# Kernel tuning notes

Hardware: AMD Instinct MI355X
Metric: run time of the kernel (lower is better)

Reference implementation:

```python
import jax, jax.numpy as jnp
import numpy as np
import math

B, LQ, D = 4, 1024, 2048
H, G = 16, 4            # n_heads, n_groups
HD = D // H             # 128
GS = H // G             # group_size = 4
PAST = 1024
LK = PAST + LQ
NEG = jnp.float32(-1e30)


def _rope(x, cos, sin):
    # x: [B, L, nh, HD]; cos/sin: [1, L, 1, HD//2]; llama-style complex rotation
    x1 = x[..., 0::2]
    x2 = x[..., 1::2]
    r1 = x1 * cos - x2 * sin
    r2 = x1 * sin + x2 * cos
    return jnp.stack([r1, r2], axis=-1).reshape(x.shape)


def setup_inputs() -> dict:
    key = jax.random.key(0)
    ks = jax.random.split(key, 12)
    s = 0.02
    x = jax.random.normal(ks[0], (B, LQ, D), jnp.float32)
    past_k = jax.random.normal(ks[1], (B, G, PAST, HD), jnp.float32)
    past_v = jax.random.normal(ks[2], (B, G, PAST, HD), jnp.float32)
    rotary_freqs = jax.random.uniform(ks[3], (LQ, HD // 2), jnp.float32) * 6.283
    # causal mask with cache: query i may attend to key j if j <= PAST + i
    q_pos = PAST + jnp.arange(LQ)[:, None]
    k_pos = jnp.arange(LK)[None, :]
    mask = (k_pos <= q_pos)  # [LQ, LK] bool
    Wq = jax.random.normal(ks[4], (D, D), jnp.float32) * s
    bq = jnp.zeros((D,), jnp.float32)
    Wk = jax.random.normal(ks[5], (D, G * HD), jnp.float32) * s
    bk = jnp.zeros((G * HD,), jnp.float32)
    Wv = jax.random.normal(ks[6], (D, G * HD), jnp.float32) * s
    bv = jnp.zeros((G * HD,), jnp.float32)
    Wo = jax.random.normal(ks[7], (D, D), jnp.float32) * s
    bo = jnp.zeros((D,), jnp.float32)
    return {"x": x, "mask": mask, "rotary_freqs": rotary_freqs,
            "past_k": past_k, "past_v": past_v,
            "Wq": Wq, "bq": bq, "Wk": Wk, "bk": bk,
            "Wv": Wv, "bv": bv, "Wo": Wo, "bo": bo}


def reference(x, mask, rotary_freqs, past_k, past_v, Wq, bq, Wk, bk, Wv, bv, Wo, bo):
    # projections (torch Linear math with weights stored [in, out])
    q = (x @ Wq + bq).reshape(B, LQ, H, HD)      # break_heads: [B,L,H,HD]
    k = (x @ Wk + bk).reshape(B, LQ, G, HD)      # [B,L,G,HD]
    v = (x @ Wv + bv).reshape(B, LQ, G, HD).transpose(0, 2, 1, 3)  # [B,G,L,HD]
    # RoPE on q,k then move heads forward (matches q.transpose(2,1))
    cos = jnp.cos(rotary_freqs)[None, :, None, :]
    sin = jnp.sin(rotary_freqs)[None, :, None, :]
    q = _rope(q, cos, sin).transpose(0, 2, 1, 3)  # [B,H,LQ,HD]
    k = _rope(k, cos, sin).transpose(0, 2, 1, 3)  # [B,G,LQ,HD]
    # KV cache append
    k = jnp.concatenate([past_k, k], axis=2)      # [B,G,LK,HD]
    v = jnp.concatenate([past_v, v], axis=2)
    # grouped-query attention
    qg = q.reshape(B, G, GS, LQ, HD)
    scores = jnp.einsum('bgsqd,bgkd->bgsqk', qg, k) / math.sqrt(HD)
    scores = jnp.where(mask[None, None, None, :, :], scores, NEG)
    att = jax.nn.softmax(scores, axis=-1)
    out = jnp.einsum('bgsqk,bgkd->bgsqd', att, v).reshape(B, H, LQ, HD)
    out = out.transpose(0, 2, 1, 3).reshape(B, LQ, D)  # concatenate_heads
    return out @ Wo + bo
```

## Files before the change

kernel.cpp:

```cpp
#include <hip/hip_runtime.h>

#define B_   4
#define LQ_  1024
#define D_   2048
#define H_   16
#define G_   4
#define HD_  128
#define GS_  4
#define PAST_ 1024
#define LK_  2048
#define NQKV 3072

typedef __attribute__((ext_vector_type(8))) short short8;
typedef __attribute__((ext_vector_type(4))) float f32x4;

__device__ __forceinline__ ushort f2b(float f) {
    unsigned u = __builtin_bit_cast(unsigned, f);
    u += 0x7FFF + ((u >> 16) & 1);
    return (ushort)(u >> 16);
}
__device__ __forceinline__ float b2f(ushort h) {
    unsigned u = ((unsigned)h) << 16;
    return __builtin_bit_cast(float, u);
}

#define GLD_LDS16(gp, lp) \
    __builtin_amdgcn_global_load_lds((__attribute__((address_space(1))) void*)(gp), \
                                     (__attribute__((address_space(3))) void*)(lp), 16, 0, 0)

__global__ __launch_bounds__(256) void prep_misc(const float* __restrict__ x,
                                                 ushort* __restrict__ xb,
                                                 const float* __restrict__ pk,
                                                 ushort* __restrict__ kc,
                                                 const float* __restrict__ bq,
                                                 const float* __restrict__ bk,
                                                 const float* __restrict__ bv,
                                                 float* __restrict__ bias) {
    int blk = blockIdx.x;
    int tid = threadIdx.x;
    if (blk < 8192) {
        int i = blk * 256 + tid;
        float4 v = ((const float4*)x)[i];
        ushort4 o;
        o.x = f2b(v.x); o.y = f2b(v.y); o.z = f2b(v.z); o.w = f2b(v.w);
        ((ushort4*)xb)[i] = o;
    } else if (blk < 10240) {
        int i = (blk - 8192) * 256 + tid;
        float4 v = ((const float4*)pk)[i];
        int bg  = i >> 15;
        int rem = i & 32767;
        ushort4 o;
        o.x = f2b(v.x); o.y = f2b(v.y); o.z = f2b(v.z); o.w = f2b(v.w);
        ((ushort4*)kc)[(size_t)bg * 65536 + rem] = o;
    } else {
        int i = (blk - 10240) * 256 + tid;
        if (i < 2048) bias[i] = bq[i];
        else if (i < 2560) bias[i] = bk[i - 2048];
        else if (i < 3072) bias[i] = bv[i - 2560];
    }
}

__global__ __launch_bounds__(256) void transpose_pack(const float* __restrict__ in,
                                                      ushort* __restrict__ out,
                                                      int rows_in, int cols_in,
                                                      long in_bstride, long out_bstride,
                                                      int out_rstride) {
    __shared__ float t[32][33];
    int bz = blockIdx.z;
    in  += (long)bz * in_bstride;
    out += (long)bz * out_bstride;
    int c0 = blockIdx.x * 32, r0 = blockIdx.y * 32;
    int tx = threadIdx.x, ty = threadIdx.y;
    #pragma unroll
    for (int i = 0; i < 32; i += 8) {
        int r = r0 + ty + i;
        if (r < rows_in && (c0 + tx) < cols_in)
            t[ty + i][tx] = in[(long)r * cols_in + c0 + tx];
    }
    __syncthreads();
    #pragma unroll
    for (int i = 0; i < 32; i += 8) {
        int c = c0 + ty + i, r = r0 + tx;
        if (c < cols_in && r < rows_in)
            out[(long)c * out_rstride + r] = f2b(t[tx][ty + i]);
    }
}

template <bool BF16_OUT>
__global__ __launch_bounds__(512, 2) void gemm256(const ushort* __restrict__ Ap,
                                                  const ushort* __restrict__ Bp,
                                                  const float* __restrict__ bias,
                                                  void* __restrict__ Cout,
                                                  int M, int N, int K) {
    __shared__ ushort sh[65536];
    const int tid = threadIdx.x;
    const int w = tid >> 6, lane = tid & 63;
    const int quad = lane >> 4, l15 = lane & 15;
    const int wr = w >> 2, wc = w & 3;
    const int m0 = blockIdx.y * 256, n0 = blockIdx.x * 256;

    const int u0 = w * 64 + lane, u1 = (8 + w) * 64 + lane;
    const int r0_ = u0 >> 3, s0_ = u0 & 7;
    const int r1_ = u1 >> 3, s1_ = u1 & 7;
    const int sw0 = (s0_ ^ (r0_ & 7)) << 3, sw1 = (s1_ ^ (r1_ & 7)) << 3;
    const int srcA00 = (m0 + r0_) * K + sw0;
    const int srcA01 = (m0 + r1_) * K + sw1;
    const int srcA10 = (m0 + 128 + r0_) * K + sw0;
    const int srcA11 = (m0 + 128 + r1_) * K + sw1;
    const int srcB00 = (n0 + r0_) * K + sw0;
    const int srcB01 = (n0 + r1_) * K + sw1;
    const int srcB10 = (n0 + 128 + r0_) * K + sw0;
    const int srcB11 = (n0 + 128 + r1_) * K + sw1;

#define STAGE_A0(t, bufx) do { ushort* d_ = sh + (bufx) * 32768 + w * 512; \
    GLD_LDS16(Ap + (size_t)(srcA00 + (t) * 64), d_); \
    GLD_LDS16(Ap + (size_t)(srcA01 + (t) * 64), d_ + 4096); } while (0)
#define STAGE_A1(t, bufx) do { ushort* d_ = sh + (bufx) * 32768 + 8192 + w * 512; \
    GLD_LDS16(Ap + (size_t)(srcA10 + (t) * 64), d_); \
    GLD_LDS16(Ap + (size_t)(srcA11 + (t) * 64), d_ + 4096); } while (0)
#define STAGE_B0(t, bufx) do { ushort* d_ = sh + (bufx) * 32768 + 16384 + w * 512; \
    GLD_LDS16(Bp + (size_t)(srcB00 + (t) * 64), d_); \
    GLD_LDS16(Bp + (size_t)(srcB01 + (t) * 64), d_ + 4096); } while (0)
#define STAGE_B1(t, bufx) do { ushort* d_ = sh + (bufx) * 32768 + 16384 + 8192 + w * 512; \
    GLD_LDS16(Bp + (size_t)(srcB10 + (t) * 64), d_); \
    GLD_LDS16(Bp + (size_t)(srcB11 + (t) * 64), d_ + 4096); } while (0)

#define READ_A(QR) \
    _Pragma("unroll") for (int fi = 0; fi < 4; ++fi) \
    _Pragma("unroll") for (int ks = 0; ks < 2; ++ks) \
        a[fi * 2 + ks] = *(const short8*)(Ab + (wr * 128 + (QR) * 64 + fi * 16 + l15) * 64 + \
                                          (((ks * 4 + quad) ^ (l15 & 7)) << 3));
#define READ_B(QC, BREG) \
    _Pragma("unroll") for (int fj = 0; fj < 2; ++fj) \
    _Pragma("unroll") for (int ks = 0; ks < 2; ++ks) \
        BREG[fj * 2 + ks] = *(const short8*)(Bb + (wc * 64 + (QC) * 32 + fj * 16 + l15) * 64 + \
                                             (((ks * 4 + quad) ^ (l15 & 7)) << 3));
#define MFMA_Q(QR, QC, BREG) \
    _Pragma("unroll") for (int ks = 0; ks < 2; ++ks) \
    _Pragma("unroll") for (int fj = 0; fj < 2; ++fj) \
    _Pragma("unroll") for (int fi = 0; fi < 4; ++fi) \
        acc[(QR) * 4 + fi][(QC) * 2 + fj] = __builtin_amdgcn_mfma_f32_16x16x32_bf16( \
            a[fi * 2 + ks], BREG[fj * 2 + ks], acc[(QR) * 4 + fi][(QC) * 2 + fj], 0, 0, 0);

#define PH_MID() do { asm volatile("" ::: "memory"); __builtin_amdgcn_s_barrier(); \
    asm volatile("s_waitcnt lgkmcnt(0)" ::: "memory"); __builtin_amdgcn_sched_barrier(0); \
    __builtin_amdgcn_s_setprio(1); } while (0)
#define PH_END() do { __builtin_amdgcn_s_setprio(0); asm volatile("" ::: "memory"); \
    __builtin_amdgcn_s_barrier(); asm volatile("" ::: "memory"); } while (0)

    f32x4 acc[8][4];
    #pragma unroll
    for (int i = 0; i < 8; ++i)
        #pragma unroll
        for (int j = 0; j < 4; ++j)
            #pragma unroll
            for (int r = 0; r < 4; ++r) acc[i][j][r] = 0.f;

    const int KT = K >> 6;

    STAGE_A0(0, 0); STAGE_A1(0, 0); STAGE_B0(0, 0); STAGE_B1(0, 0);
    STAGE_B0(1, 1); STAGE_B1(1, 1);
    asm volatile("s_waitcnt vmcnt(4)" ::: "memory");
    asm volatile("" ::: "memory");
    __builtin_amdgcn_s_barrier();
    asm volatile("" ::: "memory");

    short8 a[8], b0[4], b1[4];
    for (int t = 0; t < KT; ++t) {
        const int buf = t & 1;
        const ushort* Ab = sh + buf * 32768;
        const ushort* Bb = Ab + 16384;

        READ_A(0)
        READ_B(0, b0)
        if (t + 1 < KT) STAGE_A0(t + 1, buf ^ 1);
        PH_MID();
        MFMA_Q(0, 0, b0)
        PH_END();

        READ_B(1, b1)
        if (t + 1 < KT) STAGE_A1(t + 1, buf ^ 1);
        PH_MID();
        MFMA_Q(0, 1, b1)
        PH_END();

        READ_A(1)
        if (t + 2 < KT) STAGE_B0(t + 2, buf);
        PH_MID();
        MFMA_Q(1, 0, b0)
        PH_END();

        if (t + 2 < KT) {
            STAGE_B1(t + 2, buf);
            asm volatile("s_waitcnt vmcnt(4)" ::: "memory");
        } else {
            asm volatile("s_waitcnt vmcnt(0)" ::: "memory");
        }
        PH_MID();
        MFMA_Q(1, 1, b1)
        PH_END();
    }

    #pragma unroll
    for (int fi = 0; fi < 8; ++fi)
        #pragma unroll
        for (int fj = 0; fj < 4; ++fj)
            #pragma unroll
            for (int r = 0; r < 4; ++r) {
                int row = m0 + wr * 128 + fi * 16 + quad * 4 + r;
                int col = n0 + wc * 64 + fj * 16 + l15;
                float v = acc[fi][fj][r] + bias[col];
                if (BF16_OUT) ((ushort*)Cout)[(size_t)row * N + col] = f2b(v);
                else          ((float*)Cout)[(size_t)row * N + col] = v;
            }
#undef STAGE_A0
#undef STAGE_A1
#undef STAGE_B0
#undef STAGE_B1
#undef READ_A
#undef READ_B
#undef MFMA_Q
#undef PH_MID
#undef PH_END
}

__global__ __launch_bounds__(256) void rope_pack(const ushort* __restrict__ qkvb,
                                                 const float* __restrict__ rf,
                                                 ushort* __restrict__ qb,
                                                 ushort* __restrict__ kc,
                                                 ushort* __restrict__ vtc) {
    const float SC = 0.08838834764831845f;
    int row = blockIdx.x;
    int b = row >> 10, qi = row & 1023;
    int tid = threadIdx.x;
    const ushort* src = qkvb + (size_t)row * NQKV;

    for (int p = tid; p < 1024; p += 256) {
        int h = p >> 6, i = p & 63;
        float fr = rf[qi * 64 + i];
        float s, c; __sincosf(fr, &s, &c);
        uint pr = *(const uint*)(src + h * 128 + 2 * i);
        float x1 = b2f((ushort)(pr & 0xffff));
        float x2 = b2f((ushort)(pr >> 16));
        float r1 = (x1 * c - x2 * s) * SC;
        float r2 = (x1 * s + x2 * c) * SC;
        size_t o = (((size_t)(b * H_ + h)) * LQ_ + qi) * HD_ + 2 * i;
        *(uint*)(qb + o) = (uint)f2b(r1) | ((uint)f2b(r2) << 16);
    }
    {
        int g = tid >> 6, i = tid & 63;
        float fr = rf[qi * 64 + i];
        float s, c; __sincosf(fr, &s, &c);
        uint pr = *(const uint*)(src + 2048 + g * 128 + 2 * i);
        float x1 = b2f((ushort)(pr & 0xffff));
        float x2 = b2f((ushort)(pr >> 16));
        float r1 = x1 * c - x2 * s;
        float r2 = x1 * s + x2 * c;
        size_t o = (((size_t)(b * G_ + g)) * LK_ + PAST_ + qi) * HD_ + 2 * i;
        *(uint*)(kc + o) = (uint)f2b(r1) | ((uint)f2b(r2) << 16);
    }
    for (int e = tid; e < 512; e += 256) {
        int g = e >> 7, d = e & 127;
        vtc[(((size_t)(b * G_ + g)) * HD_ + d) * LK_ + PAST_ + qi] = src[2560 + e];
    }
}

__global__ __launch_bounds__(256, 2) void attn_kernel(const ushort* __restrict__ qb,
                                                      const ushort* __restrict__ kc,
                                                      const ushort* __restrict__ vtc,
                                                      ushort* __restrict__ attn_a) {
    __shared__ ushort kt[2][64 * 128];
    __shared__ ushort vtt[2][128 * 64];
    __shared__ ushort pt[128 * 64];

    const int tid = threadIdx.x;
    const int wave = tid >> 6, lane = tid & 63;
    const int quad = lane >> 4, l15 = lane & 15;
    const int qh = wave >> 1;
    const int jw = wave & 1;
    const int tile = (blockIdx.y < 32) ? blockIdx.x : (7 - (int)blockIdx.x);
    const int q0 = tile << 7;
    const int bh = blockIdx.y;
    const int b = bh >> 4, h = bh & 15, g = h >> 2;
    const ushort* kcb = kc + ((size_t)(b * G_ + g)) * LK_ * HD_;
    const ushort* vcb = vtc + ((size_t)(b * G_ + g)) * HD_ * LK_;

    int ksrc[4], vsrc[4];
    #pragma unroll
    for (int i = 0; i < 4; ++i) {
        int u = (wave * 4 + i) * 64 + lane;
        int key = u >> 4, cs = u & 15;
        ksrc[i] = key * HD_ + ((cs ^ (key & 15)) << 3);
        int d = u >> 3, c2 = u & 7;
        vsrc[i] = d * LK_ + ((c2 ^ (d & 7)) << 3);
    }

    short8 qf[4][4];
    #pragma unroll
    for (int qfr = 0; qfr < 4; ++qfr) {
        int qrow = q0 + qh * 64 + qfr * 16 + l15;
        const ushort* qp = qb + (((size_t)(b * H_ + h)) * LQ_ + qrow) * HD_ + quad * 8;
        #pragma unroll
        for (int kk = 0; kk < 4; ++kk) qf[qfr][kk] = *(const short8*)(qp + kk * 32);
    }

    f32x4 o[4][4];
    #pragma unroll
    for (int qfr = 0; qfr < 4; ++qfr)
        #pragma unroll
        for (int f = 0; f < 4; ++f)
            #pragma unroll
            for (int r = 0; r < 4; ++r) o[qfr][f][r] = 0.f;
    float lst[4][4];
    #pragma unroll
    for (int qfr = 0; qfr < 4; ++qfr)
        #pragma unroll
        for (int r = 0; r < 4; ++r) lst[qfr][r] = 0.f;

    const int nsteps = (PAST_ + q0 + 128) >> 6;

    #pragma unroll
    for (int i = 0; i < 4; ++i) {
        int ci = wave * 4 + i;
        GLD_LDS16(kcb + ksrc[i], kt[0] + ci * 512);
        GLD_LDS16(vcb + vsrc[i], vtt[0] + ci * 512);
    }

    for (int it = 0; it < nsteps; ++it) {
        const int k0 = it << 6;
        const int cur = it & 1, nxt = cur ^ 1;
        __syncthreads();
        if (it + 1 < nsteps) {
            const int k1 = k0 + 64;
            #pragma unroll
            for (int i = 0; i < 4; ++i) {
                int ci = wave * 4 + i;
                GLD_LDS16(kcb + (size_t)k1 * HD_ + ksrc[i], kt[nxt] + ci * 512);
                GLD_LDS16(vcb + k1 + vsrc[i], vtt[nxt] + ci * 512);
            }
        }

        f32x4 z[4][2];
        #pragma unroll
        for (int qfr = 0; qfr < 4; ++qfr)
            #pragma unroll
            for (int kf = 0; kf < 2; ++kf)
                #pragma unroll
                for (int r = 0; r < 4; ++r) z[qfr][kf][r] = 0.f;
        __builtin_amdgcn_s_setprio(1);
        #pragma unroll
        for (int kk = 0; kk < 4; ++kk) {
            #pragma unroll
            for (int kf = 0; kf < 2; ++kf) {
                int key = jw * 32 + kf * 16 + l15;
                const short8 bk = *(const short8*)(kt[cur] + key * 128 + (((kk * 4 + quad) ^ l15) << 3));
                #pragma unroll
                for (int qfr = 0; qfr < 4; ++qfr)
                    z[qfr][kf] = __builtin_amdgcn_mfma_f32_16x16x32_bf16(qf[qfr][kk], bk, z[qfr][kf], 0, 0, 0);
            }
        }
        __builtin_amdgcn_s_setprio(0);

        const bool mask_step = (it >= nsteps - 2);
        #pragma unroll
        for (int qfr = 0; qfr < 4; ++qfr) {
            #pragma unroll
            for (int kf = 0; kf < 2; ++kf) {
                #pragma unroll
                for (int r = 0; r < 4; ++r) {
                    int row = qh * 64 + qfr * 16 + quad * 4 + r;
                    int col = jw * 32 + kf * 16 + l15;
                    float pv_ = __expf(z[qfr][kf][r]);
                    if (mask_step) {
                        int qpos = PAST_ + q0 + row;
                        if (k0 + col > qpos) pv_ = 0.f;
                    }
                    lst[qfr][r] += pv_;
                    pt[row * 64 + ((((col >> 3) ^ (row & 7)) << 3) | (col & 7))] = f2b(pv_);
                }
            }
        }

        asm volatile("s_waitcnt lgkmcnt(0)" ::: "memory");
        __builtin_amdgcn_s_barrier();
        __builtin_amdgcn_sched_barrier(0);

        __builtin_amdgcn_s_setprio(1);
        #pragma unroll
        for (int j2 = 0; j2 < 2; ++j2) {
            short8 pa[4];
            #pragma unroll
            for (int qfr = 0; qfr < 4; ++qfr) {
                int prow = qh * 64 + qfr * 16 + l15;
                pa[qfr] = *(const short8*)(pt + prow * 64 + (((j2 * 4 + quad) ^ (prow & 7)) << 3));
            }
            #pragma unroll
            for (int f = 0; f < 4; ++f) {
                int d = jw * 64 + f * 16 + l15;
                const short8 bv = *(const short8*)(vtt[cur] + d * 64 + (((j2 * 4 + quad) ^ (l15 & 7)) << 3));
                #pragma unroll
                for (int qfr = 0; qfr < 4; ++qfr)
                    o[qfr][f] = __builtin_amdgcn_mfma_f32_16x16x32_bf16(pa[qfr], bv, o[qfr][f], 0, 0, 0);
            }
        }
        __builtin_amdgcn_s_setprio(0);
    }

    __syncthreads();
    float* scr = (float*)pt;
    #pragma unroll
    for (int qfr = 0; qfr < 4; ++qfr)
        #pragma unroll
        for (int r = 0; r < 4; ++r)
            scr[wave * 1024 + (qfr * 4 + r) * 64 + lane] = lst[qfr][r];
    __syncthreads();
    #pragma unroll
    for (int qfr = 0; qfr < 4; ++qfr) {
        float linv[4];
        #pragma unroll
        for (int r = 0; r < 4; ++r) {
            float rs = lst[qfr][r] + scr[(wave ^ 1) * 1024 + (qfr * 4 + r) * 64 + lane];
            rs += __shfl_xor(rs, 1);
            rs += __shfl_xor(rs, 2);
            rs += __shfl_xor(rs, 4);
            rs += __shfl_xor(rs, 8);
            linv[r] = 1.0f / rs;
        }
        #pragma unroll
        for (int f = 0; f < 4; ++f)
            #pragma unroll
            for (int r = 0; r < 4; ++r) {
                int q = q0 + qh * 64 + qfr * 16 + quad * 4 + r;
                int d = jw * 64 + f * 16 + l15;
                attn_a[((size_t)(b * LQ_ + q)) * D_ + h * HD_ + d] = f2b(o[qfr][f][r] * linv[r]);
            }
    }
}


extern "C" void kernel_launch(void* const* d_in, const int* in_sizes, int n_in,
                              void* d_out, int out_size, void* d_ws, size_t ws_size,
                              hipStream_t stream) {
    const float* x  = (const float*)d_in[0];
    const float* rf = (const float*)d_in[2];
    const float* pk = (const float*)d_in[3];
    const float* pv = (const float*)d_in[4];
    const float* Wq = (const float*)d_in[5];
    const float* bq = (const float*)d_in[6];
    const float* Wk = (const float*)d_in[7];
    const float* bk = (const float*)d_in[8];
    const float* Wv = (const float*)d_in[9];
    const float* bv = (const float*)d_in[10];
    const float* Wo = (const float*)d_in[11];
    const float* bo = (const float*)d_in[12];
    float* out = (float*)d_out;

    char* p = (char*)d_ws;
    auto take = [&](size_t n) { void* r = p; p += (n + 255) & ~(size_t)255; return r; };
    ushort* xb       = (ushort*)take((size_t)4096 * 2048 * 2);
    ushort* wt_qkv   = (ushort*)take((size_t)3072 * 2048 * 2);
    ushort* wt_o     = (ushort*)take((size_t)2048 * 2048 * 2);
    float*  bias_qkv = (float*) take((size_t)3072 * 4);
    ushort* qkvb     = (ushort*)take((size_t)4096 * 3072 * 2);
    ushort* qb       = (ushort*)take((size_t)B_ * H_ * LQ_ * HD_ * 2);
    ushort* kcache   = (ushort*)take((size_t)B_ * G_ * LK_ * HD_ * 2);
    ushort* vtc      = (ushort*)take((size_t)B_ * G_ * HD_ * LK_ * 2);
    ushort* attn_a   = (ushort*)take((size_t)4096 * 2048 * 2);

    dim3 tb(32, 8);
    prep_misc<<<10252, 256, 0, stream>>>(x, xb, pk, kcache, bq, bk, bv, bias_qkv);
    transpose_pack<<<dim3(64, 64, 1), tb, 0, stream>>>(Wq, wt_qkv, 2048, 2048, 0, 0, 2048);
    transpose_pack<<<dim3(16, 64, 1), tb, 0, stream>>>(Wk, wt_qkv + (size_t)2048 * 2048, 2048, 512, 0, 0, 2048);
    transpose_pack<<<dim3(16, 64, 1), tb, 0, stream>>>(Wv, wt_qkv + (size_t)2560 * 2048, 2048, 512, 0, 0, 2048);
    transpose_pack<<<dim3(64, 64, 1), tb, 0, stream>>>(Wo, wt_o, 2048, 2048, 0, 0, 2048);
    transpose_pack<<<dim3(4, 32, 16), tb, 0, stream>>>(pv, vtc, 1024, 128,
                                                       (long)1024 * 128, (long)128 * 2048, 2048);

    gemm256<true><<<dim3(12, 16), 512, 0, stream>>>(xb, wt_qkv, bias_qkv, qkvb, 4096, 3072, 2048);
    rope_pack<<<4096, 256, 0, stream>>>(qkvb, rf, qb, kcache, vtc);
    attn_kernel<<<dim3(8, 64), 256, 0, stream>>>(qb, kcache, vtc, attn_a);
    gemm256<false><<<dim3(8, 16), 512, 0, stream>>>(attn_a, wt_o, bo, out, 4096, 2048, 2048);
}
```

Baseline: 399.0 us.

## Split V transpose into tiled kernel, transpose score MFMA, swap output GEMM

The strided V-transpose scatter moves out of rope_pack into a dedicated LDS-tiled transpose kernel, which should give coalesced writes. The attention score MFMA swaps its operands so each lane holds four consecutive keys for one query row. That lets P be written to LDS as packed 8-byte stores and reduces the row-sum bookkeeping to one accumulator per fragment. The output projection moves from the tuned 256x256 pipelined GEMM to a new simple 128x128 GEMM with 256 threads. That GEMM has no double buffering or LDS swizzle, which risks bank conflicts and exposed load latency.

```diff
diff --git a/kernel.cpp b/kernel.cpp
--- a/kernel.cpp
+++ b/kernel.cpp
@@ -86,6 +86,85 @@
     }
 }
 
+__global__ __launch_bounds__(256) void vtrans(const ushort* __restrict__ qkvb,
+                                              ushort* __restrict__ vtc) {
+    __shared__ ushort t[64][70];
+    const int bg = blockIdx.z;
+    const int b = bg >> 2, g = bg & 3;
+    const int d0 = blockIdx.x * 64, q0 = blockIdx.y * 64;
+    const int tx = threadIdx.x, ty = threadIdx.y;
+    const ushort* src = qkvb + (size_t)(b * 1024 + q0) * NQKV + 2560 + g * 128 + d0;
+    #pragma unroll
+    for (int i = 0; i < 64; i += 4)
+        t[ty + i][tx] = src[(size_t)(ty + i) * NQKV + tx];
+    __syncthreads();
+    ushort* dst = vtc + ((size_t)bg * 128 + d0) * LK_ + PAST_ + q0;
+    #pragma unroll
+    for (int i = 0; i < 64; i += 4)
+        dst[(size_t)(ty + i) * LK_ + tx] = t[tx][ty + i];
+}
+
+template <bool BF16_OUT>
+__global__ __launch_bounds__(256) void gemm_bt(const ushort* __restrict__ A,
+                                               const ushort* __restrict__ Bt,
+                                               const float* __restrict__ bias,
+                                               void* __restrict__ Cout,
+                                               int M, int N, int K) {
+    __shared__ ushort lA[128 * 32];
+    __shared__ ushort lB[128 * 32];
+    const int tid = threadIdx.x;
+    const int wave = tid >> 6, lane = tid & 63;
+    const int quad = lane >> 4, l15 = lane & 15;
+    const int m0 = blockIdx.y * 128, n0 = blockIdx.x * 128;
+    const int wm = (wave >> 1) * 64, wn = (wave & 1) * 64;
+
+    f32x4 acc[4][4];
+    #pragma unroll
+    for (int i = 0; i < 4; ++i)
+        #pragma unroll
+        for (int j = 0; j < 4; ++j)
+            #pragma unroll
+            for (int r = 0; r < 4; ++r) acc[i][j][r] = 0.f;
+
+    for (int k0 = 0; k0 < K; k0 += 32) {
+        __syncthreads();
+        #pragma unroll
+        for (int i = 0; i < 2; ++i) {
+            int chunk = wave * 2 + i;
+            int flat = chunk * 512 + lane * 8;
+            int row = flat >> 5, col = flat & 31;
+            GLD_LDS16(A  + (size_t)(m0 + row) * K + k0 + col, lA + chunk * 512);
+            GLD_LDS16(Bt + (size_t)(n0 + row) * K + k0 + col, lB + chunk * 512);
+        }
+        __syncthreads();
+        short8 af[4], bf[4];
+        #pragma unroll
+        for (int i = 0; i < 4; ++i)
+            af[i] = *(const short8*)(lA + (wm + i * 16 + l15) * 32 + quad * 8);
+        #pragma unroll
+        for (int j = 0; j < 4; ++j)
+            bf[j] = *(const short8*)(lB + (wn + j * 16 + l15) * 32 + quad * 8);
+        #pragma unroll
+        for (int i = 0; i < 4; ++i)
+            #pragma unroll
+            for (int j = 0; j < 4; ++j)
+                acc[i][j] = __builtin_amdgcn_mfma_f32_16x16x32_bf16(af[i], bf[j], acc[i][j], 0, 0, 0);
+    }
+
+    #pragma unroll
+    for (int i = 0; i < 4; ++i)
+        #pragma unroll
+        for (int j = 0; j < 4; ++j)
+            #pragma unroll
+            for (int r = 0; r < 4; ++r) {
+                int row = m0 + wm + i * 16 + quad * 4 + r;
+                int col = n0 + wn + j * 16 + l15;
+                float v = acc[i][j][r] + bias[col];
+                if (BF16_OUT) ((ushort*)Cout)[(size_t)row * N + col] = f2b(v);
+                else          ((float*)Cout)[(size_t)row * N + col] = v;
+            }
+}
+
 template <bool BF16_OUT>
 __global__ __launch_bounds__(512, 2) void gemm256(const ushort* __restrict__ Ap,
                                                   const ushort* __restrict__ Bp,
@@ -227,8 +306,7 @@
 __global__ __launch_bounds__(256) void rope_pack(const ushort* __restrict__ qkvb,
                                                  const float* __restrict__ rf,
                                                  ushort* __restrict__ qb,
-                                                 ushort* __restrict__ kc,
-                                                 ushort* __restrict__ vtc) {
+                                                 ushort* __restrict__ kc) {
     const float SC = 0.08838834764831845f;
     int row = blockIdx.x;
     int b = row >> 10, qi = row & 1023;
@@ -259,10 +337,6 @@
         size_t o = (((size_t)(b * G_ + g)) * LK_ + PAST_ + qi) * HD_ + 2 * i;
         *(uint*)(kc + o) = (uint)f2b(r1) | ((uint)f2b(r2) << 16);
     }
-    for (int e = tid; e < 512; e += 256) {
-        int g = e >> 7, d = e & 127;
-        vtc[(((size_t)(b * G_ + g)) * HD_ + d) * LK_ + PAST_ + qi] = src[2560 + e];
-    }
 }
 
 __global__ __launch_bounds__(256, 2) void attn_kernel(const ushort* __restrict__ qb,
@@ -311,11 +385,9 @@
         for (int f = 0; f < 4; ++f)
             #pragma unroll
             for (int r = 0; r < 4; ++r) o[qfr][f][r] = 0.f;
-    float lst[4][4];
-    #pragma unroll
-    for (int qfr = 0; qfr < 4; ++qfr)
-        #pragma unroll
-        for (int r = 0; r < 4; ++r) lst[qfr][r] = 0.f;
+    float lstq[4];
+    #pragma unroll
+    for (int qfr = 0; qfr < 4; ++qfr) lstq[qfr] = 0.f;
 
     const int nsteps = (PAST_ + q0 + 128) >> 6;
 
@@ -356,7 +428,7 @@
                 const short8 bk = *(const short8*)(kt[cur] + key * 128 + (((kk * 4 + quad) ^ l15) << 3));
                 #pragma unroll
                 for (int qfr = 0; qfr < 4; ++qfr)
-                    z[qfr][kf] = __builtin_amdgcn_mfma_f32_16x16x32_bf16(qf[qfr][kk], bk, z[qfr][kf], 0, 0, 0);
+                    z[qfr][kf] = __builtin_amdgcn_mfma_f32_16x16x32_bf16(bk, qf[qfr][kk], z[qfr][kf], 0, 0, 0);
             }
         }
         __builtin_amdgcn_s_setprio(0);
@@ -364,20 +436,26 @@
         const bool mask_step = (it >= nsteps - 2);
         #pragma unroll
         for (int qfr = 0; qfr < 4; ++qfr) {
+            const int row = qh * 64 + qfr * 16 + l15;
             #pragma unroll
             for (int kf = 0; kf < 2; ++kf) {
+                float pv0[4];
                 #pragma unroll
                 for (int r = 0; r < 4; ++r) {
-                    int row = qh * 64 + qfr * 16 + quad * 4 + r;
-                    int col = jw * 32 + kf * 16 + l15;
                     float pv_ = __expf(z[qfr][kf][r]);
                     if (mask_step) {
-                        int qpos = PAST_ + q0 + row;
-                        if (k0 + col > qpos) pv_ = 0.f;
+                        int keyg = k0 + jw * 32 + kf * 16 + quad * 4 + r;
+                        if (keyg > PAST_ + q0 + row) pv_ = 0.f;
                     }
-                    lst[qfr][r] += pv_;
-                    pt[row * 64 + ((((col >> 3) ^ (row & 7)) << 3) | (col & 7))] = f2b(pv_);
+                    lstq[qfr] += pv_;
+                    pv0[r] = pv_;
                 }
+                uint2 val;
+                val.x = (uint)f2b(pv0[0]) | ((uint)f2b(pv0[1]) << 16);
+                val.y = (uint)f2b(pv0[2]) | ((uint)f2b(pv0[3]) << 16);
+                int unit = jw * 4 + kf * 2 + (quad >> 1);
+                int swz = ((unit ^ (row & 7)) << 3) + ((quad & 1) << 2);
+                *(uint2*)(pt + row * 64 + swz) = val;
             }
         }
 
@@ -406,26 +484,27 @@
         __builtin_amdgcn_s_setprio(0);
     }
 
+    float rq[4];
+    #pragma unroll
+    for (int qfr = 0; qfr < 4; ++qfr) {
+        float rs = lstq[qfr];
+        rs += __shfl_xor(rs, 16);
+        rs += __shfl_xor(rs, 32);
+        rq[qfr] = rs;
+    }
     __syncthreads();
     float* scr = (float*)pt;
     #pragma unroll
     for (int qfr = 0; qfr < 4; ++qfr)
+        scr[wave * 256 + qfr * 64 + lane] = rq[qfr];
+    __syncthreads();
+    #pragma unroll
+    for (int qfr = 0; qfr < 4; ++qfr) {
+        float tot = rq[qfr] + scr[(wave ^ 1) * 256 + qfr * 64 + lane];
+        float linv[4];
         #pragma unroll
         for (int r = 0; r < 4; ++r)
-            scr[wave * 1024 + (qfr * 4 + r) * 64 + lane] = lst[qfr][r];
-    __syncthreads();
-    #pragma unroll
-    for (int qfr = 0; qfr < 4; ++qfr) {
-        float linv[4];
-        #pragma unroll
-        for (int r = 0; r < 4; ++r) {
-            float rs = lst[qfr][r] + scr[(wave ^ 1) * 1024 + (qfr * 4 + r) * 64 + lane];
-            rs += __shfl_xor(rs, 1);
-            rs += __shfl_xor(rs, 2);
-            rs += __shfl_xor(rs, 4);
-            rs += __shfl_xor(rs, 8);
-            linv[r] = 1.0f / rs;
-        }
+            linv[r] = 1.0f / __shfl(tot, quad * 4 + r, 16);
         #pragma unroll
         for (int f = 0; f < 4; ++f)
             #pragma unroll
@@ -477,7 +556,8 @@
                                                        (long)1024 * 128, (long)128 * 2048, 2048);
 
     gemm256<true><<<dim3(12, 16), 512, 0, stream>>>(xb, wt_qkv, bias_qkv, qkvb, 4096, 3072, 2048);
-    rope_pack<<<4096, 256, 0, stream>>>(qkvb, rf, qb, kcache, vtc);
+    rope_pack<<<4096, 256, 0, stream>>>(qkvb, rf, qb, kcache);
+    vtrans<<<dim3(2, 16, 16), dim3(64, 4), 0, stream>>>(qkvb, vtc);
     attn_kernel<<<dim3(8, 64), 256, 0, stream>>>(qb, kcache, vtc, attn_a);
-    gemm256<false><<<dim3(8, 16), 512, 0, stream>>>(attn_a, wt_o, bo, out, 4096, 2048, 2048);
-}
+    gemm_bt<false><<<dim3(16, 32), 256, 0, stream>>>(attn_a, wt_o, bo, out, 4096, 2048, 2048);
+}
```

Result: faster. 378.3 us (-5.2%).
